# Kernel optimization log

Hardware: AMD Instinct MI355X
Metric: run time of the kernel (lower is better)

Reference implementation:

```python
import jax, jax.numpy as jnp
import numpy as np

EPS_LN = 1e-6  # ieps_ln_default


def setup_inputs() -> dict:
    key = jax.random.key(0)
    ks = jax.random.split(key, 8)
    B, S, H, ID = 8, 2048, 8, 256  # batch, seq, heads, i_head_dim
    OD = 256                        # o_head_dim
    sc_hid = 1.0 / np.sqrt(2 * ID)
    sc_og = 1.0 / np.sqrt(ID + OD)
    return {
        "heads_input": jax.random.normal(ks[0], (B, S, H, ID), dtype=jnp.float32),
        "W_hid": jax.random.uniform(ks[1], (3 * OD, 2 * ID), jnp.float32, -sc_hid, sc_hid),
        "b_hid": jnp.zeros((3 * OD,), jnp.float32),
        "W_og": jax.random.uniform(ks[2], (OD, ID + OD), jnp.float32, -sc_og, sc_og),
        "b_og": jnp.zeros((OD,), jnp.float32),
        "ln_w": jnp.ones((H, ID), jnp.float32),
        "ln_b": jnp.zeros((H, ID), jnp.float32),
        "init_cx": jnp.zeros((H, OD), jnp.float32),
    }


def _forward(heads_input, W_hid, b_hid, W_og, b_og, ln_w, ln_b, init_cx):
    B, S, H, ID = heads_input.shape
    OD = init_cx.shape[-1]
    # RS1cumsumstatnorm: causal running sum, LayerNorm over (heads, dim) jointly
    csum = jnp.cumsum(heads_input, axis=1)
    mean = jnp.mean(csum, axis=(-2, -1), keepdims=True)
    var = jnp.var(csum, axis=(-2, -1), keepdims=True)
    csum = (csum - mean) * jax.lax.rsqrt(var + EPS_LN) * ln_w + ln_b
    # trans_hid on cat(input, csum): [B,S,H,2*ID] -> [B,S,H,3*OD]
    x2 = jnp.concatenate([heads_input, csum], axis=-1)
    g = jnp.einsum('bshd,od->bsho', x2, W_hid) + b_hid
    g = g.reshape(B, S, H, 3, OD)
    igate, fgate, hidden = g[..., 0, :], g[..., 1, :], g[..., 2, :]
    fgate = jax.nn.sigmoid(fgate)
    igh = jax.nn.sigmoid(igate) * jax.nn.relu(hidden)
    # LGateFunc: cell_t = f_t * cell_{t-1} + igh_t, starting from init_cx
    c0 = jnp.broadcast_to(init_cx, (B, H, OD))

    def step(c, fi):
        f, ig = fi
        c = f * c + ig
        return c, c

    _, cells = jax.lax.scan(step, c0, (jnp.moveaxis(fgate, 1, 0), jnp.moveaxis(igh, 1, 0)))
    cell = jnp.moveaxis(cells, 0, 1)  # [B,S,H,OD]
    # output gate on cat(input, cell)
    xo = jnp.concatenate([heads_input, cell], axis=-1)
    og = jax.nn.sigmoid(jnp.einsum('bshd,od->bsho', xo, W_og) + b_og)
    return og * cell


def reference(heads_input, W_hid, b_hid, W_og, b_og, ln_w, ln_b, init_cx):
    return _forward(heads_input, W_hid, b_hid, W_og, b_og, ln_w, ln_b, init_cx)
```

## Files before the change

### kernel.cpp

```cpp
#include <hip/hip_runtime.h>

typedef unsigned short u16;
typedef unsigned int u32;

typedef __attribute__((ext_vector_type(8))) short bf16x8;
typedef __attribute__((ext_vector_type(4))) float f32x4;

#define B_ 8
#define S_ 2048
#define H_ 8
#define ID_ 256
#define OD_ 256
#define K_ 512
#define M_ (B_*S_*H_)
#define N1_ 768
#define N2_ 256

#define CSCH 64
#define CSST (S_/CSCH)

#define OFF_X2   (0ull)
#define SZ_X2    ((unsigned long long)M_*K_*2)
#define OFF_G    (OFF_X2 + SZ_X2)
#define SZ_G     ((unsigned long long)M_*N1_*2)
#define OFF_WH   (OFF_G + SZ_G)
#define SZ_WH    ((unsigned long long)N1_*K_*2)
#define OFF_WO   (OFF_WH + SZ_WH)
#define SZ_WO    ((unsigned long long)N2_*K_*2)
#define OFF_AUX  (OFF_WO + SZ_WO)
#define SZ_AUX   ((unsigned long long)B_*CSCH*2048*4)
#define OFF_CF   (OFF_AUX + SZ_AUX)
#define SZ_CARR  ((unsigned long long)B_*H_*32*256*4)
#define OFF_CC   (OFF_CF + SZ_CARR)
#define OFF_CIN  (OFF_CC + SZ_CARR)

__device__ __forceinline__ u16 f2bf(float f) {
    union { float f; u32 u; } v; v.f = f;
    u32 u = v.u;
    u += 0x7fffu + ((u >> 16) & 1u);
    return (u16)(u >> 16);
}
__device__ __forceinline__ float bf2f(u16 h) {
    union { u32 u; float f; } v; v.u = ((u32)h) << 16;
    return v.f;
}
__device__ __forceinline__ float sigm(float x) {
    return 1.0f / (1.0f + __expf(-x));
}

__device__ __forceinline__ void gld16(const void* g, void* l) {
    __builtin_amdgcn_global_load_lds(
        (const __attribute__((address_space(1))) void*)g,
        (__attribute__((address_space(3))) void*)l, 16, 0, 0);
}

__global__ __launch_bounds__(256) void wconv_kernel(
    const float* __restrict__ Whid, const float* __restrict__ Wog,
    u16* __restrict__ WhB, u16* __restrict__ WoB)
{
    int idx = blockIdx.x * 256 + threadIdx.x;
    if (idx < N1_*K_) WhB[idx] = f2bf(Whid[idx]);
    if (idx < N2_*K_) WoB[idx] = f2bf(Wog[idx]);
}

__global__ __launch_bounds__(256) void csum_phase1(
    const float* __restrict__ X, float* __restrict__ aux)
{
    const int bch = blockIdx.x;
    const int b = bch / CSCH, ch = bch % CSCH;
    const int t = threadIdx.x;
    float acc[8];
#pragma unroll
    for (int h = 0; h < 8; ++h) acc[h] = 0.f;
    for (int i = 0; i < CSST; ++i) {
        const int s = ch * CSST + i;
        const float* xp = X + ((size_t)(b * S_ + s)) * 2048 + t;
#pragma unroll
        for (int h = 0; h < 8; ++h) acc[h] += xp[h * 256];
    }
    float* ap = aux + (size_t)bch * 2048 + t;
#pragma unroll
    for (int h = 0; h < 8; ++h) ap[h * 256] = acc[h];
}

__global__ __launch_bounds__(256) void csum_mid(float* __restrict__ aux)
{
    const int idx = blockIdx.x * 256 + threadIdx.x;
    const int b = idx >> 11, c = idx & 2047;
    float run = 0.f;
    for (int ch = 0; ch < CSCH; ++ch) {
        float* p = aux + ((size_t)(b * CSCH + ch)) * 2048 + c;
        float v = *p; *p = run; run += v;
    }
}

__global__ __launch_bounds__(256) void csum_phase2(
    const float* __restrict__ X, const float* __restrict__ aux,
    const float* __restrict__ lnw, const float* __restrict__ lnb,
    u16* __restrict__ x2)
{
    const int bch = blockIdx.x;
    const int b = bch / CSCH, ch = bch % CSCH;
    const int t = threadIdx.x;
    float c[8], wv[8], bv[8];
#pragma unroll
    for (int h = 0; h < 8; ++h) {
        c[h]  = aux[(size_t)bch * 2048 + h * 256 + t];
        wv[h] = lnw[h * 256 + t];
        bv[h] = lnb[h * 256 + t];
    }
    __shared__ float red[2][4];
    for (int i = 0; i < CSST; ++i) {
        const int s = ch * CSST + i;
        const float* xp = X + ((size_t)(b * S_ + s)) * 2048 + t;
        float xa[8];
#pragma unroll
        for (int h = 0; h < 8; ++h) { xa[h] = xp[h * 256]; c[h] += xa[h]; }
        float sx = 0.f, sq = 0.f;
#pragma unroll
        for (int h = 0; h < 8; ++h) { sx += c[h]; sq += c[h] * c[h]; }
#pragma unroll
        for (int off = 32; off >= 1; off >>= 1) {
            sx += __shfl_down(sx, (unsigned)off);
            sq += __shfl_down(sq, (unsigned)off);
        }
        const int wid = t >> 6;
        if ((t & 63) == 0) { red[0][wid] = sx; red[1][wid] = sq; }
        __syncthreads();
        const float tsx = red[0][0] + red[0][1] + red[0][2] + red[0][3];
        const float tsq = red[1][0] + red[1][1] + red[1][2] + red[1][3];
        __syncthreads();
        const float mean = tsx * (1.f / 2048.f);
        const float var  = tsq * (1.f / 2048.f) - mean * mean;
        const float rstd = rsqrtf(var + 1e-6f);
        const size_t mrow = ((size_t)(b * S_ + s)) * H_;
#pragma unroll
        for (int h = 0; h < 8; ++h) {
            u16* row = x2 + (mrow + h) * (size_t)K_;
            row[t]       = f2bf(xa[h]);
            row[256 + t] = f2bf((c[h] - mean) * rstd * wv[h] + bv[h]);
        }
    }
}

template<int N, bool OG_EPI>
__global__ __launch_bounds__(256) void gemm_kernel(
    const u16* __restrict__ A, const u16* __restrict__ Bw,
    u16* __restrict__ Gout, const float* __restrict__ bias,
    const u16* __restrict__ cellbuf, float* __restrict__ Out)
{
    constexpr int NT = N / 128;
    const int blk = blockIdx.x;
    const int xcd = blk & 7;
    const int j = blk >> 3;
    const int tileN = j % NT;
    const int tileM = (j / NT) * 8 + xcd;
    const int m0 = tileM * 128, n0 = tileN * 128;
    const int tid = threadIdx.x;
    const int lane = tid & 63;
    const int w = tid >> 6, wm = w & 1, wn = w >> 1;
    const int l15 = lane & 15, quad = lane >> 4;

    __shared__ __align__(16) u16 smem[2 * 128 * 64];
    u16* As = smem;
    u16* Bs = smem + 128 * 64;

    const int lane3 = lane >> 3;
    const int pc = lane & 7;
    const int ra7 = l15 & 7;

    f32x4 acc[4][4];
    const f32x4 zero4 = {0.f, 0.f, 0.f, 0.f};
#pragma unroll
    for (int i = 0; i < 4; ++i)
#pragma unroll
        for (int jj = 0; jj < 4; ++jj) acc[i][jj] = zero4;

    for (int kt = 0; kt < K_ / 64; ++kt) {
        const int k0 = kt * 64;
#pragma unroll
        for (int p = 0; p < 4; ++p) {
            const int R0 = w * 32 + p * 8;
            const int r = R0 + lane3;
            const int ca = (pc ^ (r & 7)) * 8;
            gld16(A  + (size_t)(m0 + r) * K_ + k0 + ca, As + R0 * 64);
            gld16(Bw + (size_t)(n0 + r) * K_ + k0 + ca, Bs + R0 * 64);
        }
        asm volatile("s_waitcnt vmcnt(0)" ::: "memory");
        __syncthreads();
#pragma unroll
        for (int kk = 0; kk < 2; ++kk) {
            bf16x8 af[4], bfr[4];
#pragma unroll
            for (int i = 0; i < 4; ++i) {
                const int rowa = wm * 64 + i * 16 + l15;
                const int rowb = wn * 64 + i * 16 + l15;
                const int ca = ((kk * 4 + quad) ^ ra7) * 8;
                af[i]  = *(const bf16x8*)(const void*)(&As[rowa * 64 + ca]);
                bfr[i] = *(const bf16x8*)(const void*)(&Bs[rowb * 64 + ca]);
            }
#pragma unroll
            for (int i = 0; i < 4; ++i)
#pragma unroll
                for (int jj = 0; jj < 4; ++jj)
                    acc[i][jj] = __builtin_amdgcn_mfma_f32_16x16x32_bf16(
                        af[i], bfr[jj], acc[i][jj], 0, 0, 0);
        }
        __syncthreads();
    }

    if (!OG_EPI) {
        u16* Cs = smem;
#pragma unroll
        for (int i = 0; i < 4; ++i) {
            const int lrow0 = wm * 64 + i * 16 + quad * 4;
#pragma unroll
            for (int jj = 0; jj < 4; ++jj) {
                const int col = wn * 64 + jj * 16 + l15;
#pragma unroll
                for (int r = 0; r < 4; ++r)
                    Cs[(lrow0 + r) * 128 + col] = f2bf(acc[i][jj][r]);
            }
        }
        __syncthreads();
#pragma unroll
        for (int p = 0; p < 8; ++p) {
            const int row = p * 16 + (tid >> 4);
            const int ch16 = tid & 15;
            uint4 v = *(const uint4*)(const void*)(&Cs[row * 128 + ch16 * 8]);
            *(uint4*)(void*)(Gout + (size_t)(m0 + row) * N + n0 + ch16 * 8) = v;
        }
    } else {
        float* Cf = (float*)smem;
        const int col4 = (tid & 31) * 4;
        float4 b4 = *(const float4*)(const void*)(bias + n0 + col4);
#pragma unroll
        for (int half = 0; half < 2; ++half) {
            if (wm == half) {
#pragma unroll
                for (int i = 0; i < 4; ++i) {
                    const int lrow0 = i * 16 + quad * 4;
#pragma unroll
                    for (int jj = 0; jj < 4; ++jj) {
                        const int col = wn * 64 + jj * 16 + l15;
#pragma unroll
                        for (int r = 0; r < 4; ++r)
                            Cf[(lrow0 + r) * 128 + col] = acc[i][jj][r];
                    }
                }
            }
            __syncthreads();
#pragma unroll
            for (int q = 0; q < 8; ++q) {
                const int lrow = q * 8 + (tid >> 5);
                const int grow = m0 + half * 64 + lrow;
                float4 v = *(const float4*)(const void*)(&Cf[lrow * 128 + col4]);
                const u16* cp = cellbuf + (size_t)grow * K_ + 256 + n0 + col4;
                float4 o;
                o.x = sigm(v.x + b4.x) * bf2f(cp[0]);
                o.y = sigm(v.y + b4.y) * bf2f(cp[1]);
                o.z = sigm(v.z + b4.z) * bf2f(cp[2]);
                o.w = sigm(v.w + b4.w) * bf2f(cp[3]);
                *(float4*)(void*)(Out + (size_t)grow * N2_ + n0 + col4) = o;
            }
            __syncthreads();
        }
    }
}

__global__ __launch_bounds__(256) void scan_phase1(
    const u16* __restrict__ g, const float* __restrict__ bhid,
    float* __restrict__ cF, float* __restrict__ cC)
{
    const int blk = blockIdx.x;
    const int chp = blk & 15, bh = blk >> 4;
    const int h = bh & 7, b = bh >> 3;
    const int t = threadIdx.x;
    const int ch = chp * 2 + (t >> 7);
    const int o = (t & 127) * 2;
    const float bi0 = bhid[o],       bi1 = bhid[o + 1];
    const float bf0 = bhid[256 + o], bf1 = bhid[257 + o];
    const float bh0 = bhid[512 + o], bh1 = bhid[513 + o];
    float F0 = 1.f, F1 = 1.f, c0 = 0.f, c1 = 0.f;
    for (int i = 0; i < 64; ++i) {
        const int s = ch * 64 + i;
        const size_t m = ((size_t)(b * S_ + s)) * H_ + h;
        const u16* gp = g + m * N1_;
        const u32 igp = *(const u32*)(const void*)(gp + o);
        const u32 fgp = *(const u32*)(const void*)(gp + 256 + o);
        const u32 hdp = *(const u32*)(const void*)(gp + 512 + o);
        const float f0 = sigm(bf2f((u16)fgp) + bf0);
        const float f1 = sigm(bf2f((u16)(fgp >> 16)) + bf1);
        const float i0 = sigm(bf2f((u16)igp) + bi0) * fmaxf(bf2f((u16)hdp) + bh0, 0.f);
        const float i1 = sigm(bf2f((u16)(igp >> 16)) + bi1) * fmaxf(bf2f((u16)(hdp >> 16)) + bh1, 0.f);
        c0 = f0 * c0 + i0;  F0 *= f0;
        c1 = f1 * c1 + i1;  F1 *= f1;
    }
    const size_t idx = ((size_t)(bh * 32 + ch)) * 256 + o;
    cF[idx] = F0; cF[idx + 1] = F1;
    cC[idx] = c0; cC[idx + 1] = c1;
}

__global__ __launch_bounds__(256) void scan_mid(
    const float* __restrict__ cF, const float* __restrict__ cC,
    const float* __restrict__ initcx, float* __restrict__ cin)
{
    const int bh = blockIdx.x;
    const int h = bh & 7;
    const int o = threadIdx.x;
    float c = initcx[h * 256 + o];
    for (int ch = 0; ch < 32; ++ch) {
        const size_t idx = ((size_t)(bh * 32 + ch)) * 256 + o;
        cin[idx] = c;
        c = cF[idx] * c + cC[idx];
    }
}

__global__ __launch_bounds__(256) void scan_phase2(
    const u16* __restrict__ g, const float* __restrict__ bhid,
    const float* __restrict__ cin, u16* __restrict__ x2)
{
    const int blk = blockIdx.x;
    const int chp = blk & 15, bh = blk >> 4;
    const int h = bh & 7, b = bh >> 3;
    const int t = threadIdx.x;
    const int ch = chp * 2 + (t >> 7);
    const int o = (t & 127) * 2;
    const float bi0 = bhid[o],       bi1 = bhid[o + 1];
    const float bf0 = bhid[256 + o], bf1 = bhid[257 + o];
    const float bh0 = bhid[512 + o], bh1 = bhid[513 + o];
    const size_t idx = ((size_t)(bh * 32 + ch)) * 256 + o;
    float c0 = cin[idx], c1 = cin[idx + 1];
    for (int i = 0; i < 64; ++i) {
        const int s = ch * 64 + i;
        const size_t m = ((size_t)(b * S_ + s)) * H_ + h;
        const u16* gp = g + m * N1_;
        const u32 igp = *(const u32*)(const void*)(gp + o);
        const u32 fgp = *(const u32*)(const void*)(gp + 256 + o);
        const u32 hdp = *(const u32*)(const void*)(gp + 512 + o);
        const float f0 = sigm(bf2f((u16)fgp) + bf0);
        const float f1 = sigm(bf2f((u16)(fgp >> 16)) + bf1);
        const float i0 = sigm(bf2f((u16)igp) + bi0) * fmaxf(bf2f((u16)hdp) + bh0, 0.f);
        const float i1 = sigm(bf2f((u16)(igp >> 16)) + bi1) * fmaxf(bf2f((u16)(hdp >> 16)) + bh1, 0.f);
        c0 = f0 * c0 + i0;
        c1 = f1 * c1 + i1;
        const u32 pk = (u32)f2bf(c0) | ((u32)f2bf(c1) << 16);
        *(u32*)(void*)(x2 + m * K_ + 256 + o) = pk;
    }
}

extern "C" void kernel_launch(void* const* d_in, const int* in_sizes, int n_in,
                              void* d_out, int out_size, void* d_ws, size_t ws_size,
                              hipStream_t stream)
{
    const float* X      = (const float*)d_in[0];
    const float* Whid   = (const float*)d_in[1];
    const float* bhid   = (const float*)d_in[2];
    const float* Wog    = (const float*)d_in[3];
    const float* bog    = (const float*)d_in[4];
    const float* lnw    = (const float*)d_in[5];
    const float* lnb    = (const float*)d_in[6];
    const float* initcx = (const float*)d_in[7];
    float* out = (float*)d_out;

    char* ws = (char*)d_ws;
    u16* x2   = (u16*)(ws + OFF_X2);
    u16* g    = (u16*)(ws + OFF_G);
    u16* WhB  = (u16*)(ws + OFF_WH);
    u16* WoB  = (u16*)(ws + OFF_WO);
    float* aux = (float*)(ws + OFF_AUX);
    float* cF  = (float*)(ws + OFF_CF);
    float* cC  = (float*)(ws + OFF_CC);
    float* cin = (float*)(ws + OFF_CIN);

    wconv_kernel<<<(N1_*K_ + 255) / 256, 256, 0, stream>>>(Whid, Wog, WhB, WoB);
    csum_phase1<<<B_ * CSCH, 256, 0, stream>>>(X, aux);
    csum_mid<<<64, 256, 0, stream>>>(aux);
    csum_phase2<<<B_ * CSCH, 256, 0, stream>>>(X, aux, lnw, lnb, x2);
    gemm_kernel<N1_, false><<<(M_ / 128) * (N1_ / 128), 256, 0, stream>>>(
        x2, WhB, g, nullptr, nullptr, nullptr);
    scan_phase1<<<B_ * H_ * 16, 256, 0, stream>>>(g, bhid, cF, cC);
    scan_mid<<<B_ * H_, 256, 0, stream>>>(cF, cC, initcx, cin);
    scan_phase2<<<B_ * H_ * 16, 256, 0, stream>>>(g, bhid, cin, x2);
    gemm_kernel<N2_, true><<<(M_ / 128) * (N2_ / 128), 256, 0, stream>>>(
        x2, WoB, nullptr, bog, x2, out);
}
```

Measured before the change: 642.3 us.

## Fuse gate activations into first GEMM epilogue and store compact fp16 gates

Permutes W_hid rows so that input-gate and hidden columns interleave inside each 128-wide tile. The first GEMM epilogue can then compute sigmoid(i)*relu(h) and sigmoid(f) and write a 512-wide fp16 gate buffer instead of the 768-wide raw bf16 output. The scan kernels read this smaller precomputed buffer with 4-wide vector loads, removing the redundant activation work in both scan passes and a third of the intermediate traffic. The trade-offs are fp16 precision for the gates and extra transcendental work in the GEMM epilogue.

```diff
diff --git a/kernel.cpp b/kernel.cpp
--- a/kernel.cpp
+++ b/kernel.cpp
@@ -15,6 +15,7 @@
 #define M_ (B_*S_*H_)
 #define N1_ 768
 #define N2_ 256
+#define G2_ 512
 
 #define CSCH 64
 #define CSST (S_/CSCH)
@@ -22,7 +23,7 @@
 #define OFF_X2   (0ull)
 #define SZ_X2    ((unsigned long long)M_*K_*2)
 #define OFF_G    (OFF_X2 + SZ_X2)
-#define SZ_G     ((unsigned long long)M_*N1_*2)
+#define SZ_G     ((unsigned long long)M_*G2_*2)
 #define OFF_WH   (OFF_G + SZ_G)
 #define SZ_WH    ((unsigned long long)N1_*K_*2)
 #define OFF_WO   (OFF_WH + SZ_WH)
@@ -33,6 +34,8 @@
 #define SZ_CARR  ((unsigned long long)B_*H_*32*256*4)
 #define OFF_CC   (OFF_CF + SZ_CARR)
 #define OFF_CIN  (OFF_CC + SZ_CARR)
+#define OFF_BR   (OFF_CIN + SZ_CARR)
+#define SZ_BR    ((unsigned long long)N1_*4)
 
 __device__ __forceinline__ u16 f2bf(float f) {
     union { float f; u32 u; } v; v.f = f;
@@ -44,6 +47,15 @@
     union { u32 u; float f; } v; v.u = ((u32)h) << 16;
     return v.f;
 }
+__device__ __forceinline__ u32 pack2h(float a, float b) {
+    union { _Float16 h; u16 u; } x, y;
+    x.h = (_Float16)a; y.h = (_Float16)b;
+    return (u32)x.u | ((u32)y.u << 16);
+}
+__device__ __forceinline__ float h2f(u16 u) {
+    union { u16 u; _Float16 h; } v; v.u = u;
+    return (float)v.h;
+}
 __device__ __forceinline__ float sigm(float x) {
     return 1.0f / (1.0f + __expf(-x));
 }
@@ -54,13 +66,26 @@
         (__attribute__((address_space(3))) void*)l, 16, 0, 0);
 }
 
+__device__ __forceinline__ int whid_src_row(int n) {
+    if (n < 512) {
+        int o = ((n >> 7) << 6) + ((n & 127) >> 1);
+        return (n & 1) ? (512 + o) : o;
+    }
+    return 256 + (n - 512);
+}
+
 __global__ __launch_bounds__(256) void wconv_kernel(
-    const float* __restrict__ Whid, const float* __restrict__ Wog,
-    u16* __restrict__ WhB, u16* __restrict__ WoB)
+    const float* __restrict__ Whid, const float* __restrict__ bhid,
+    const float* __restrict__ Wog,
+    u16* __restrict__ WhB, u16* __restrict__ WoB, float* __restrict__ br)
 {
     int idx = blockIdx.x * 256 + threadIdx.x;
-    if (idx < N1_*K_) WhB[idx] = f2bf(Whid[idx]);
+    if (idx < N1_*K_) {
+        const int n = idx >> 9, k = idx & 511;
+        WhB[idx] = f2bf(Whid[(size_t)whid_src_row(n) * K_ + k]);
+    }
     if (idx < N2_*K_) WoB[idx] = f2bf(Wog[idx]);
+    if (idx < N1_) br[idx] = bhid[whid_src_row(idx)];
 }
 
 __global__ __launch_bounds__(256) void csum_phase1(
@@ -143,7 +168,7 @@
     }
 }
 
-template<int N, bool OG_EPI>
+template<int N, int EPI>
 __global__ __launch_bounds__(256) void gemm_kernel(
     const u16* __restrict__ A, const u16* __restrict__ Bw,
     u16* __restrict__ Gout, const float* __restrict__ bias,
@@ -209,52 +234,46 @@
         __syncthreads();
     }
 
-    if (!OG_EPI) {
-        u16* Cs = smem;
-#pragma unroll
-        for (int i = 0; i < 4; ++i) {
-            const int lrow0 = wm * 64 + i * 16 + quad * 4;
-#pragma unroll
-            for (int jj = 0; jj < 4; ++jj) {
-                const int col = wn * 64 + jj * 16 + l15;
-#pragma unroll
-                for (int r = 0; r < 4; ++r)
-                    Cs[(lrow0 + r) * 128 + col] = f2bf(acc[i][jj][r]);
-            }
-        }
-        __syncthreads();
-#pragma unroll
-        for (int p = 0; p < 8; ++p) {
-            const int row = p * 16 + (tid >> 4);
-            const int ch16 = tid & 15;
-            uint4 v = *(const uint4*)(const void*)(&Cs[row * 128 + ch16 * 8]);
-            *(uint4*)(void*)(Gout + (size_t)(m0 + row) * N + n0 + ch16 * 8) = v;
-        }
-    } else {
-        float* Cf = (float*)smem;
-        const int col4 = (tid & 31) * 4;
-        float4 b4 = *(const float4*)(const void*)(bias + n0 + col4);
-#pragma unroll
-        for (int half = 0; half < 2; ++half) {
-            if (wm == half) {
-#pragma unroll
-                for (int i = 0; i < 4; ++i) {
-                    const int lrow0 = i * 16 + quad * 4;
-#pragma unroll
-                    for (int jj = 0; jj < 4; ++jj) {
-                        const int col = wn * 64 + jj * 16 + l15;
-#pragma unroll
-                        for (int r = 0; r < 4; ++r)
-                            Cf[(lrow0 + r) * 128 + col] = acc[i][jj][r];
-                    }
+    float* Cf = (float*)smem;
+    const int col4 = (tid & 31) * 4;
+    float4 b4;
+    if (EPI == 0) b4 = *(const float4*)(const void*)(bias + n0 + col4);
+    else          b4 = *(const float4*)(const void*)(bias + n0 + col4);
+#pragma unroll
+    for (int half = 0; half < 2; ++half) {
+        if (wm == half) {
+#pragma unroll
+            for (int i = 0; i < 4; ++i) {
+                const int lrow0 = i * 16 + quad * 4;
+#pragma unroll
+                for (int jj = 0; jj < 4; ++jj) {
+                    const int col = wn * 64 + jj * 16 + l15;
+#pragma unroll
+                    for (int r = 0; r < 4; ++r)
+                        Cf[(lrow0 + r) * 128 + col] = acc[i][jj][r];
                 }
             }
-            __syncthreads();
-#pragma unroll
-            for (int q = 0; q < 8; ++q) {
-                const int lrow = q * 8 + (tid >> 5);
-                const int grow = m0 + half * 64 + lrow;
-                float4 v = *(const float4*)(const void*)(&Cf[lrow * 128 + col4]);
+        }
+        __syncthreads();
+#pragma unroll
+        for (int q = 0; q < 8; ++q) {
+            const int lrow = q * 8 + (tid >> 5);
+            const int grow = m0 + half * 64 + lrow;
+            float4 v = *(const float4*)(const void*)(&Cf[lrow * 128 + col4]);
+            if (EPI == 0) {
+                if (tileN < 4) {
+                    const float ig0 = sigm(v.x + b4.x) * fmaxf(v.y + b4.y, 0.f);
+                    const float ig1 = sigm(v.z + b4.z) * fmaxf(v.w + b4.w, 0.f);
+                    *(u32*)(void*)(Gout + (size_t)grow * G2_ + tileN * 64 + (col4 >> 1))
+                        = pack2h(ig0, ig1);
+                } else {
+                    uint2 pk;
+                    pk.x = pack2h(sigm(v.x + b4.x), sigm(v.y + b4.y));
+                    pk.y = pack2h(sigm(v.z + b4.z), sigm(v.w + b4.w));
+                    *(uint2*)(void*)(Gout + (size_t)grow * G2_ + 256 + (tileN - 4) * 128 + col4)
+                        = pk;
+                }
+            } else {
                 const u16* cp = cellbuf + (size_t)grow * K_ + 256 + n0 + col4;
                 float4 o;
                 o.x = sigm(v.x + b4.x) * bf2f(cp[0]);
@@ -263,42 +282,38 @@
                 o.w = sigm(v.w + b4.w) * bf2f(cp[3]);
                 *(float4*)(void*)(Out + (size_t)grow * N2_ + n0 + col4) = o;
             }
-            __syncthreads();
-        }
+        }
+        __syncthreads();
     }
 }
 
 __global__ __launch_bounds__(256) void scan_phase1(
-    const u16* __restrict__ g, const float* __restrict__ bhid,
-    float* __restrict__ cF, float* __restrict__ cC)
+    const u16* __restrict__ g2, float* __restrict__ cF, float* __restrict__ cC)
 {
     const int blk = blockIdx.x;
-    const int chp = blk & 15, bh = blk >> 4;
+    const int chp = blk & 7, bh = blk >> 3;
     const int h = bh & 7, b = bh >> 3;
     const int t = threadIdx.x;
-    const int ch = chp * 2 + (t >> 7);
-    const int o = (t & 127) * 2;
-    const float bi0 = bhid[o],       bi1 = bhid[o + 1];
-    const float bf0 = bhid[256 + o], bf1 = bhid[257 + o];
-    const float bh0 = bhid[512 + o], bh1 = bhid[513 + o];
-    float F0 = 1.f, F1 = 1.f, c0 = 0.f, c1 = 0.f;
+    const int ch = chp * 4 + (t >> 6);
+    const int o = (t & 63) * 4;
+    float F[4] = {1.f, 1.f, 1.f, 1.f};
+    float c[4] = {0.f, 0.f, 0.f, 0.f};
     for (int i = 0; i < 64; ++i) {
         const int s = ch * 64 + i;
         const size_t m = ((size_t)(b * S_ + s)) * H_ + h;
-        const u16* gp = g + m * N1_;
-        const u32 igp = *(const u32*)(const void*)(gp + o);
-        const u32 fgp = *(const u32*)(const void*)(gp + 256 + o);
-        const u32 hdp = *(const u32*)(const void*)(gp + 512 + o);
-        const float f0 = sigm(bf2f((u16)fgp) + bf0);
-        const float f1 = sigm(bf2f((u16)(fgp >> 16)) + bf1);
-        const float i0 = sigm(bf2f((u16)igp) + bi0) * fmaxf(bf2f((u16)hdp) + bh0, 0.f);
-        const float i1 = sigm(bf2f((u16)(igp >> 16)) + bi1) * fmaxf(bf2f((u16)(hdp >> 16)) + bh1, 0.f);
-        c0 = f0 * c0 + i0;  F0 *= f0;
-        c1 = f1 * c1 + i1;  F1 *= f1;
+        const u16* gp = g2 + m * G2_;
+        const uint2 igp = *(const uint2*)(const void*)(gp + o);
+        const uint2 fgp = *(const uint2*)(const void*)(gp + 256 + o);
+        const float f0 = h2f((u16)fgp.x), f1 = h2f((u16)(fgp.x >> 16));
+        const float f2 = h2f((u16)fgp.y), f3 = h2f((u16)(fgp.y >> 16));
+        c[0] = f0 * c[0] + h2f((u16)igp.x);        F[0] *= f0;
+        c[1] = f1 * c[1] + h2f((u16)(igp.x >> 16)); F[1] *= f1;
+        c[2] = f2 * c[2] + h2f((u16)igp.y);        F[2] *= f2;
+        c[3] = f3 * c[3] + h2f((u16)(igp.y >> 16)); F[3] *= f3;
     }
     const size_t idx = ((size_t)(bh * 32 + ch)) * 256 + o;
-    cF[idx] = F0; cF[idx + 1] = F1;
-    cC[idx] = c0; cC[idx + 1] = c1;
+    *(float4*)(void*)(cF + idx) = make_float4(F[0], F[1], F[2], F[3]);
+    *(float4*)(void*)(cC + idx) = make_float4(c[0], c[1], c[2], c[3]);
 }
 
 __global__ __launch_bounds__(256) void scan_mid(
@@ -317,35 +332,34 @@
 }
 
 __global__ __launch_bounds__(256) void scan_phase2(
-    const u16* __restrict__ g, const float* __restrict__ bhid,
-    const float* __restrict__ cin, u16* __restrict__ x2)
+    const u16* __restrict__ g2, const float* __restrict__ cin,
+    u16* __restrict__ x2)
 {
     const int blk = blockIdx.x;
-    const int chp = blk & 15, bh = blk >> 4;
+    const int chp = blk & 7, bh = blk >> 3;
     const int h = bh & 7, b = bh >> 3;
     const int t = threadIdx.x;
-    const int ch = chp * 2 + (t >> 7);
-    const int o = (t & 127) * 2;
-    const float bi0 = bhid[o],       bi1 = bhid[o + 1];
-    const float bf0 = bhid[256 + o], bf1 = bhid[257 + o];
-    const float bh0 = bhid[512 + o], bh1 = bhid[513 + o];
+    const int ch = chp * 4 + (t >> 6);
+    const int o = (t & 63) * 4;
     const size_t idx = ((size_t)(bh * 32 + ch)) * 256 + o;
-    float c0 = cin[idx], c1 = cin[idx + 1];
+    float4 c4 = *(const float4*)(const void*)(cin + idx);
+    float c[4] = {c4.x, c4.y, c4.z, c4.w};
     for (int i = 0; i < 64; ++i) {
         const int s = ch * 64 + i;
         const size_t m = ((size_t)(b * S_ + s)) * H_ + h;
-        const u16* gp = g + m * N1_;
-        const u32 igp = *(const u32*)(const void*)(gp + o);
-        const u32 fgp = *(const u32*)(const void*)(gp + 256 + o);
-        const u32 hdp = *(const u32*)(const void*)(gp + 512 + o);
-        const float f0 = sigm(bf2f((u16)fgp) + bf0);
-        const float f1 = sigm(bf2f((u16)(fgp >> 16)) + bf1);
-        const float i0 = sigm(bf2f((u16)igp) + bi0) * fmaxf(bf2f((u16)hdp) + bh0, 0.f);
-        const float i1 = sigm(bf2f((u16)(igp >> 16)) + bi1) * fmaxf(bf2f((u16)(hdp >> 16)) + bh1, 0.f);
-        c0 = f0 * c0 + i0;
-        c1 = f1 * c1 + i1;
-        const u32 pk = (u32)f2bf(c0) | ((u32)f2bf(c1) << 16);
-        *(u32*)(void*)(x2 + m * K_ + 256 + o) = pk;
+        const u16* gp = g2 + m * G2_;
+        const uint2 igp = *(const uint2*)(const void*)(gp + o);
+        const uint2 fgp = *(const uint2*)(const void*)(gp + 256 + o);
+        const float f0 = h2f((u16)fgp.x), f1 = h2f((u16)(fgp.x >> 16));
+        const float f2 = h2f((u16)fgp.y), f3 = h2f((u16)(fgp.y >> 16));
+        c[0] = f0 * c[0] + h2f((u16)igp.x);
+        c[1] = f1 * c[1] + h2f((u16)(igp.x >> 16));
+        c[2] = f2 * c[2] + h2f((u16)igp.y);
+        c[3] = f3 * c[3] + h2f((u16)(igp.y >> 16));
+        uint2 pk;
+        pk.x = (u32)f2bf(c[0]) | ((u32)f2bf(c[1]) << 16);
+        pk.y = (u32)f2bf(c[2]) | ((u32)f2bf(c[3]) << 16);
+        *(uint2*)(void*)(x2 + m * K_ + 256 + o) = pk;
     }
 }
 
@@ -372,16 +386,17 @@
     float* cF  = (float*)(ws + OFF_CF);
     float* cC  = (float*)(ws + OFF_CC);
     float* cin = (float*)(ws + OFF_CIN);
-
-    wconv_kernel<<<(N1_*K_ + 255) / 256, 256, 0, stream>>>(Whid, Wog, WhB, WoB);
+    float* br  = (float*)(ws + OFF_BR);
+
+    wconv_kernel<<<(N1_*K_ + 255) / 256, 256, 0, stream>>>(Whid, bhid, Wog, WhB, WoB, br);
     csum_phase1<<<B_ * CSCH, 256, 0, stream>>>(X, aux);
     csum_mid<<<64, 256, 0, stream>>>(aux);
     csum_phase2<<<B_ * CSCH, 256, 0, stream>>>(X, aux, lnw, lnb, x2);
-    gemm_kernel<N1_, false><<<(M_ / 128) * (N1_ / 128), 256, 0, stream>>>(
-        x2, WhB, g, nullptr, nullptr, nullptr);
-    scan_phase1<<<B_ * H_ * 16, 256, 0, stream>>>(g, bhid, cF, cC);
+    gemm_kernel<N1_, 0><<<(M_ / 128) * (N1_ / 128), 256, 0, stream>>>(
+        x2, WhB, g, br, nullptr, nullptr);
+    scan_phase1<<<B_ * H_ * 8, 256, 0, stream>>>(g, cF, cC);
     scan_mid<<<B_ * H_, 256, 0, stream>>>(cF, cC, initcx, cin);
-    scan_phase2<<<B_ * H_ * 16, 256, 0, stream>>>(g, bhid, cin, x2);
-    gemm_kernel<N2_, true><<<(M_ / 128) * (N2_ / 128), 256, 0, stream>>>(
+    scan_phase2<<<B_ * H_ * 8, 256, 0, stream>>>(g, cin, x2);
+    gemm_kernel<N2_, 1><<<(M_ / 128) * (N2_ / 128), 256, 0, stream>>>(
         x2, WoB, nullptr, bog, x2, out);
 }
```

Result: no change. 640.0 us (-0.4%).
